# Performance work log

Hardware: AMD Instinct MI355X
Metric: run time of the kernel (lower is better)

## Reference

```python
import jax, jax.numpy as jnp
import numpy as np

D = 1024
H = 16
DK = D // H

def setup_inputs() -> dict:
    key = jax.random.key(0)
    k1, k2, k3 = jax.random.split(key, 3)
    x = jax.random.normal(k1, (2, 2048, D), dtype=jnp.float32)
    # torch nn.Linear weight shapes: qkv [3D, D], o [D, D]; y = x @ W.T
    scale = 1.0 / np.sqrt(D)
    W_qkv = jax.random.normal(k2, (3 * D, D), dtype=jnp.float32) * scale
    W_o = jax.random.normal(k3, (D, D), dtype=jnp.float32) * scale
    return {"x": x, "W_qkv": W_qkv, "W_o": W_o}

def reference(x, W_qkv, W_o):
    B, T, _ = x.shape
    qkv = x @ W_qkv.T                                    # [B, T, 3D]
    qkv = qkv.reshape(B, T, 3, H, DK)
    qkv = jnp.transpose(qkv, (0, 3, 2, 1, 4))            # [B, H, 3, T, DK]
    q, k, v = qkv[:, :, 0], qkv[:, :, 1], qkv[:, :, 2]   # each [B, H, T, DK]
    scores = jnp.einsum("bhqd,bhkd->bhqk", q, k) / np.sqrt(DK)
    causal = jnp.tril(jnp.ones((T, T), dtype=bool))       # keep lower triangle
    scores = jnp.where(causal, scores, -jnp.inf)
    attn = jax.nn.softmax(scores, axis=-1)
    out = jnp.einsum("bhqk,bhkd->bhqd", attn, v)          # [B, H, T, DK]
    out = jnp.transpose(out, (0, 2, 1, 3)).reshape(B, T, H * DK)
    return out @ W_o.T
```

## Files before the change

kernel.cpp:

```cpp
#include <hip/hip_runtime.h>
#include <hip/hip_bf16.h>

typedef __bf16 bf16x8 __attribute__((ext_vector_type(8)));
typedef float f32x4 __attribute__((ext_vector_type(4)));
typedef unsigned int u32;
typedef u32 u32x4 __attribute__((ext_vector_type(4)));

#define MFMA(a, b, c) __builtin_amdgcn_mfma_f32_16x16x32_bf16((a), (b), (c), 0, 0, 0)

static __device__ __forceinline__ bf16x8 ld8(const __bf16* p) {
  return *reinterpret_cast<const bf16x8*>(p);
}

static __device__ __forceinline__ u32 pkbf(float a, float b) {
  union { __bf16 h; unsigned short s; } x, y;
  x.h = (__bf16)a; y.h = (__bf16)b;
  return (u32)x.s | ((u32)y.s << 16);
}

typedef unsigned int __attribute__((address_space(1))) gu32_t;
typedef unsigned int __attribute__((address_space(3))) lu32_t;
static __device__ __forceinline__ void gld16(const __bf16* g, __bf16* l) {
  __builtin_amdgcn_global_load_lds((const gu32_t*)(const void*)g,
                                   (lu32_t*)(void*)l, 16, 0, 0);
}

__global__ __launch_bounds__(256)
void cvt_f32_bf16(const float* __restrict__ a, __bf16* __restrict__ oa, int na,
                  const float* __restrict__ b, __bf16* __restrict__ ob) {
  const int i = blockIdx.x * 256 + threadIdx.x;
  const float* src; __bf16* dst; int e;
  if (i < (na >> 3)) { src = a; dst = oa; e = i << 3; }
  else { src = b; dst = ob; e = (i << 3) - na; }
  f32x4 v0 = *reinterpret_cast<const f32x4*>(src + e);
  f32x4 v1 = *reinterpret_cast<const f32x4*>(src + e + 4);
  bf16x8 o;
#pragma unroll
  for (int j = 0; j < 4; ++j) { o[j] = (__bf16)v0[j]; o[j + 4] = (__bf16)v1[j]; }
  *reinterpret_cast<bf16x8*>(dst + e) = o;
}

static __device__ __forceinline__ void stage8f(__bf16* __restrict__ dst,
                                               const float* __restrict__ src) {
  f32x4 a = *reinterpret_cast<const f32x4*>(src);
  f32x4 b = *reinterpret_cast<const f32x4*>(src + 4);
  bf16x8 o;
#pragma unroll
  for (int i = 0; i < 4; ++i) { o[i] = (__bf16)a[i]; o[i + 4] = (__bf16)b[i]; }
  *reinterpret_cast<bf16x8*>(dst) = o;
}

template<int BN, bool SPLIT, bool OUT_BF16, bool B_F32>
__global__ __launch_bounds__(256, 2)
void gemm3(const __bf16* __restrict__ A, const void* __restrict__ Wv,
           void* __restrict__ Cv, __bf16* __restrict__ VT,
           int M, int N, int K) {
  constexpr int NF = BN / 32;
  constexpr float SC2Q = 0.125f * 1.4426950408889634f;
  __shared__ __bf16 lA[128 * 64];
  __shared__ __bf16 lB[BN * 64];

  const int tid = threadIdx.x;
  const int ntiles = N / BN;
  const int per = gridDim.x >> 3;
  const int bid = (blockIdx.x & 7) * per + (blockIdx.x >> 3);
  const int mt = bid / ntiles;
  const int nt = bid % ntiles;
  const int m0 = mt << 7, n0 = nt * BN;
  const int lane = tid & 63, w = tid >> 6;
  const int wm = (w >> 1) << 6;
  const int wn = (w & 1) * (BN / 2);
  const int fr = lane & 15, fg = lane >> 4;

  f32x4 acc[4][NF] = {};

  for (int k0 = 0; k0 < K; k0 += 64) {
    __syncthreads();
#pragma unroll
    for (int jj = 0; jj < 4; ++jj) {
      const int q = (w << 2) | jj;
      const int v = (q << 6) | lane;
      const int row = v >> 3;
      const int cc = (v & 7) ^ (row & 7);
      gld16(A + (size_t)(m0 + row) * K + k0 + (cc << 3), lA + (q << 9));
    }
    if constexpr (B_F32) {
#pragma unroll
      for (int hh = 0; hh < BN / 64; ++hh) {
        const int row = (tid >> 2) + (hh << 6);
        const int c0 = (tid & 3) << 1;
        const float* src = (const float*)Wv + (size_t)(n0 + row) * K + k0 + (c0 << 3);
#pragma unroll
        for (int cg = 0; cg < 2; ++cg)
          stage8f(lB + (row << 6) + (((c0 + cg) ^ (row & 7)) << 3), src + (cg << 3));
      }
    } else {
#pragma unroll
      for (int jj = 0; jj < NF; ++jj) {
        const int q = w * NF + jj;
        const int v = (q << 6) | lane;
        const int row = v >> 3;
        const int cc = (v & 7) ^ (row & 7);
        gld16((const __bf16*)Wv + (size_t)(n0 + row) * K + k0 + (cc << 3), lB + (q << 9));
      }
    }
    __syncthreads();

    bf16x8 af[2][4], bfr[2][NF];
#pragma unroll
    for (int kc = 0; kc < 2; ++kc) {
#pragma unroll
      for (int m = 0; m < 4; ++m) {
        const int row = wm + m * 16 + fr;
        af[kc][m] = ld8(lA + (row << 6) + ((((kc << 2) | fg) ^ (row & 7)) << 3));
      }
#pragma unroll
      for (int n = 0; n < NF; ++n) {
        const int row = wn + n * 16 + fr;
        bfr[kc][n] = ld8(lB + (row << 6) + ((((kc << 2) | fg) ^ (row & 7)) << 3));
      }
    }
#pragma unroll
    for (int kc = 0; kc < 2; ++kc)
#pragma unroll
      for (int m = 0; m < 4; ++m)
#pragma unroll
        for (int n = 0; n < NF; ++n)
          acc[m][n] = MFMA(af[kc][m], bfr[kc][n], acc[m][n]);
  }

#pragma unroll
  for (int m = 0; m < 4; ++m) {
#pragma unroll
    for (int n = 0; n < NF; ++n) {
#pragma unroll
      for (int r = 0; r < 4; ++r) {
        int row = m0 + wm + m * 16 + fg * 4 + r;
        int col = n0 + wn + n * 16 + fr;
        float v = acc[m][n][r];
        if constexpr (SPLIT) {
          int b = row >> 11, t = row & 2047;
          if (col >= 2048) {
            VT[((size_t)(b << 10) + (col - 2048)) * 2048 + t] = (__bf16)v;
          } else {
            if (col < 1024) v *= SC2Q;
            ((__bf16*)Cv)[(size_t)row * 2048 + col] = (__bf16)v;
          }
        } else if constexpr (OUT_BF16) {
          ((__bf16*)Cv)[(size_t)row * N + col] = (__bf16)v;
        } else {
          ((float*)Cv)[(size_t)row * N + col] = v;
        }
      }
    }
  }
}

static __device__ __forceinline__ void softmax_step(
    f32x4 (&s)[4], f32x4 (&o)[4], float& m, float& l, bf16x8 (&pa)[2],
    bool diag, int q0wt, int k0, int fg, int fr) {
  constexpr float NEG = -1e30f;
  float sv[4][4];
#pragma unroll
  for (int n = 0; n < 4; ++n)
#pragma unroll
    for (int r = 0; r < 4; ++r) {
      float x = s[n][r];
      if (diag && (k0 + n * 16 + fg * 4 + r > q0wt + fr)) x = NEG;
      sv[n][r] = x;
    }

  float t0 = fmaxf(fmaxf(sv[0][0], sv[0][1]), fmaxf(sv[0][2], sv[0][3]));
  float t1 = fmaxf(fmaxf(sv[1][0], sv[1][1]), fmaxf(sv[1][2], sv[1][3]));
  float t2 = fmaxf(fmaxf(sv[2][0], sv[2][1]), fmaxf(sv[2][2], sv[2][3]));
  float t3 = fmaxf(fmaxf(sv[3][0], sv[3][1]), fmaxf(sv[3][2], sv[3][3]));
  float rm = fmaxf(fmaxf(t0, t1), fmaxf(t2, t3));
  rm = fmaxf(rm, __shfl_xor(rm, 16));
  rm = fmaxf(rm, __shfl_xor(rm, 32));

  if (!__all(rm <= m + 16.f)) {
    float mnew = fmaxf(m, rm);
    float alpha = __builtin_exp2f(m - mnew);
    m = mnew;
    l *= alpha;
    float ao[4];
#pragma unroll
    for (int r = 0; r < 4; ++r)
      ao[r] = __shfl(alpha, fg * 4 + r);
#pragma unroll
    for (int n = 0; n < 4; ++n)
#pragma unroll
      for (int r = 0; r < 4; ++r)
        o[n][r] *= ao[r];
  }

  float p[4][4];
#pragma unroll
  for (int n = 0; n < 4; ++n)
#pragma unroll
    for (int r = 0; r < 4; ++r)
      p[n][r] = __builtin_exp2f(sv[n][r] - m);

  float u0 = (p[0][0] + p[0][1]) + (p[0][2] + p[0][3]);
  float u1 = (p[1][0] + p[1][1]) + (p[1][2] + p[1][3]);
  float u2 = (p[2][0] + p[2][1]) + (p[2][2] + p[2][3]);
  float u3 = (p[3][0] + p[3][1]) + (p[3][2] + p[3][3]);
  float rs = (u0 + u1) + (u2 + u3);
  rs += __shfl_xor(rs, 16);
  rs += __shfl_xor(rs, 32);
  l += rs;

  u32 wpk[4][2];
#pragma unroll
  for (int n = 0; n < 4; ++n) {
    wpk[n][0] = pkbf(p[n][0], p[n][1]);
    wpk[n][1] = pkbf(p[n][2], p[n][3]);
  }

  u32 rcv[2][2][2];
#pragma unroll
  for (int e = 0; e < 2; ++e) {
    const int src = fr + ((((fg & 1) << 1) | ((fg >> 1) ^ e)) << 4);
    const bool tsel = ((fg & 1) ^ e) != 0;
#pragma unroll
    for (int c = 0; c < 2; ++c)
#pragma unroll
      for (int hh = 0; hh < 2; ++hh) {
        u32 v = tsel ? wpk[(c << 1) | 1][hh] : wpk[(c << 1) | 0][hh];
        rcv[e][c][hh] = (u32)__shfl((int)v, src);
      }
  }
  const bool hi = (fg >> 1) != 0;
  u32x4 w0, w1;
#pragma unroll
  for (int a = 0; a < 2; ++a)
#pragma unroll
    for (int hh = 0; hh < 2; ++hh) {
      w0[2 * a + hh] = hi ? rcv[a ^ 1][0][hh] : rcv[a][0][hh];
      w1[2 * a + hh] = hi ? rcv[a ^ 1][1][hh] : rcv[a][1][hh];
    }
  pa[0] = __builtin_bit_cast(bf16x8, w0);
  pa[1] = __builtin_bit_cast(bf16x8, w1);
}

static __device__ __forceinline__ void write_out(
    __bf16* __restrict__ out, f32x4 (&o)[4], float l,
    int b, int hoff, int q0wt, int fg, int fr) {
  float linv = 1.f / l;
  float lo[4];
#pragma unroll
  for (int r = 0; r < 4; ++r)
    lo[r] = __shfl(linv, fg * 4 + r);
#pragma unroll
  for (int n = 0; n < 4; ++n)
#pragma unroll
    for (int r = 0; r < 4; ++r) {
      int t = q0wt + fg * 4 + r;
      out[((size_t)(b * 2048 + t)) * 1024 + hoff + n * 16 + fr] = (__bf16)(o[n][r] * lo[r]);
    }
}

__global__ __launch_bounds__(256, 4)
void attn_causal10(const __bf16* __restrict__ qk, const __bf16* __restrict__ vt,
                   __bf16* __restrict__ out) {
  constexpr float NEG = -1e30f;

  __shared__ __bf16 lK[2][4096];
  __shared__ __bf16 lV[2][4096];

  const int tid = threadIdx.x;
  const int lane = tid & 63, w = tid >> 6;
  const int fr = lane & 15, fg = lane >> 4;
  const int blk = blockIdx.x;
  const int j = blk >> 3;
  const int bh = ((blk & 7) << 2) | (j & 3);
  const int qb = 31 - (j >> 2);
  const int b = bh >> 4, h = bh & 15;
  const int q0w = (qb << 6) + (w << 4);
  const int hoff = h * 64;
  const size_t qkbase = (size_t)b * (2048 * 2048);
  const __bf16* kb = qk + qkbase + 1024 + hoff;
  const __bf16* vtb = vt + (size_t)((b << 10) | hoff) * 2048;

  bf16x8 qf[2];
#pragma unroll
  for (int c = 0; c < 2; ++c)
    qf[c] = ld8(qk + qkbase + (size_t)(q0w + fr) * 2048 + hoff + c * 32 + fg * 8);

  f32x4 o[4] = {};
  float m = NEG;
  float l = 0.f;

#define STAGE(bf, k0s)                                                        \
  do {                                                                        \
    _Pragma("unroll")                                                         \
    for (int jj = 0; jj < 2; ++jj) {                                          \
      const int q = (w << 1) | jj;                                            \
      const int v = (q << 6) | lane;                                          \
      const int row = v >> 3;                                                 \
      const int cc = (v & 7) ^ (row & 7);                                     \
      gld16(kb + (size_t)((k0s) + row) * 2048 + (cc << 3), &lK[bf][q << 9]);  \
      gld16(vtb + (size_t)row * 2048 + (k0s) + (cc << 3), &lV[bf][q << 9]);   \
    }                                                                         \
  } while (0)

  int buf = 0;
  STAGE(0, 0);
  __syncthreads();

  for (int kt = 0; kt <= qb; ++kt) {
    const int k0 = kt << 6;
    if (kt < qb) STAGE(buf ^ 1, k0 + 64);

    f32x4 s[4] = {};
#pragma unroll
    for (int c = 0; c < 2; ++c) {
      bf16x8 kfc[4];
#pragma unroll
      for (int n = 0; n < 4; ++n) {
        const int row = n * 16 + fr;
        const int sc = ((c << 2) | fg) ^ (row & 7);
        kfc[n] = ld8(&lK[buf][(row << 6) + (sc << 3)]);
      }
#pragma unroll
      for (int n = 0; n < 4; ++n)
        s[n] = MFMA(kfc[n], qf[c], s[n]);
    }

    bf16x8 pa[2];
    softmax_step(s, o, m, l, pa, kt == qb, q0w, k0, fg, fr);

#pragma unroll
    for (int c = 0; c < 2; ++c) {
      bf16x8 vfc[4];
#pragma unroll
      for (int n = 0; n < 4; ++n) {
        const int row = n * 16 + fr;
        const int sc = ((c << 2) | fg) ^ (row & 7);
        vfc[n] = ld8(&lV[buf][(row << 6) + (sc << 3)]);
      }
#pragma unroll
      for (int n = 0; n < 4; ++n)
        o[n] = MFMA(pa[c], vfc[n], o[n]);
    }

    __syncthreads();
    buf ^= 1;
  }
#undef STAGE

  write_out(out, o, l, b, hoff, q0w, fg, fr);
}

extern "C" void kernel_launch(void* const* d_in, const int* in_sizes, int n_in,
                              void* d_out, int out_size, void* d_ws, size_t ws_size,
                              hipStream_t stream) {
  const float* x = (const float*)d_in[0];
  const float* w_qkv = (const float*)d_in[1];
  const float* w_o = (const float*)d_in[2];
  float* out = (float*)d_out;

  const int M = 4096;
  __bf16* qk = (__bf16*)d_ws;
  __bf16* vt = (__bf16*)((char*)d_ws + (size_t)M * 2048 * 2);
  __bf16* attn = (__bf16*)((char*)d_ws + (size_t)M * 3072 * 2);

  __bf16* xb = (__bf16*)d_out;
  __bf16* wqb = xb + 4194304;
  const int NX = 4194304;

  cvt_f32_bf16<<<3584, 256, 0, stream>>>(x, xb, NX, w_qkv, wqb);

  gemm3<128, true, true, false><<<(M / 128) * (3072 / 128), 256, 0, stream>>>(
      xb, (const void*)wqb, (void*)qk, vt, M, 3072, 1024);

  attn_causal10<<<1024, 256, 0, stream>>>(qk, vt, attn);

  gemm3<64, false, false, true><<<(M / 128) * (1024 / 64), 256, 0, stream>>>(
      attn, (const void*)w_o, (void*)out, nullptr, M, 1024, 1024);
}
```

Measured before the change: 119.3 us.

## Split longest causal query blocks across two workgroups and merge with combine kernel

The 8 heaviest query blocks per (b,h) are split into two workgroups that process interleaved (even/odd) key tiles. Each half writes a normalized partial output plus a log-sum-exp statistic, and a new combine kernel merges them with softmax weights. The goal is to shorten the critical-path tail of the causal workload and to balance work across the 1280 workgroups, and the occupancy hint is raised to 5 waves. In exchange it adds an extra kernel launch, extra global traffic for the partials, and bf16 rounding of the partial outputs before they are combined.

```diff
diff --git a/kernel.cpp b/kernel.cpp
--- a/kernel.cpp
+++ b/kernel.cpp
@@ -260,9 +260,10 @@
     }
 }
 
-__global__ __launch_bounds__(256, 4)
-void attn_causal10(const __bf16* __restrict__ qk, const __bf16* __restrict__ vt,
-                   __bf16* __restrict__ out) {
+__global__ __launch_bounds__(256, 5)
+void attn_causal16(const __bf16* __restrict__ qk, const __bf16* __restrict__ vt,
+                   __bf16* __restrict__ attn, __bf16* __restrict__ pb1,
+                   float* __restrict__ sbuf) {
   constexpr float NEG = -1e30f;
 
   __shared__ __bf16 lK[2][4096];
@@ -272,9 +273,14 @@
   const int lane = tid & 63, w = tid >> 6;
   const int fr = lane & 15, fg = lane >> 4;
   const int blk = blockIdx.x;
-  const int j = blk >> 3;
-  const int bh = ((blk & 7) << 2) | (j & 3);
-  const int qb = 31 - (j >> 2);
+  const int bh = ((blk & 7) << 2) | ((blk >> 3) & 3);
+  const int jb = blk >> 5;
+  int qb, p0, st;
+  bool split;
+  if (jb < 8) { qb = 23 - jb; p0 = 0; st = 1; split = false; }
+  else if (jb < 24) { int sj = jb - 8; qb = 31 - (sj >> 1); p0 = sj & 1; st = 2; split = true; }
+  else { qb = 15 - (jb - 24); p0 = 0; st = 1; split = false; }
+
   const int b = bh >> 4, h = bh & 15;
   const int q0w = (qb << 6) + (w << 4);
   const int hoff = h * 64;
@@ -305,12 +311,12 @@
   } while (0)
 
   int buf = 0;
-  STAGE(0, 0);
+  STAGE(0, p0 << 6);
   __syncthreads();
 
-  for (int kt = 0; kt <= qb; ++kt) {
+  for (int kt = p0; kt <= qb; kt += st) {
     const int k0 = kt << 6;
-    if (kt < qb) STAGE(buf ^ 1, k0 + 64);
+    if (kt + st <= qb) STAGE(buf ^ 1, (kt + st) << 6);
 
     f32x4 s[4] = {};
 #pragma unroll
@@ -349,7 +355,57 @@
   }
 #undef STAGE
 
-  write_out(out, o, l, b, hoff, q0w, fg, fr);
+  if (!split) {
+    write_out(attn, o, l, b, hoff, q0w, fg, fr);
+  } else {
+    const int ti = ((31 - qb) << 5) | bh;
+    const float s_stat = m + __log2f(l);
+    if (p0 == 0) {
+      write_out(attn, o, l, b, hoff, q0w, fg, fr);
+      if (fg == 0) sbuf[ti * 64 + w * 16 + fr] = s_stat;
+    } else {
+      float linv = 1.f / l;
+      float lo[4];
+#pragma unroll
+      for (int r = 0; r < 4; ++r)
+        lo[r] = __shfl(linv, fg * 4 + r);
+#pragma unroll
+      for (int n = 0; n < 4; ++n)
+#pragma unroll
+        for (int r = 0; r < 4; ++r)
+          pb1[(size_t)ti * 4096 + (w * 16 + fg * 4 + r) * 64 + n * 16 + fr] =
+              (__bf16)(o[n][r] * lo[r]);
+      if (fg == 0) sbuf[16384 + ti * 64 + w * 16 + fr] = s_stat;
+    }
+  }
+}
+
+__global__ __launch_bounds__(256)
+void attn_combine16(const __bf16* __restrict__ pb1, const float* __restrict__ sbuf,
+                    __bf16* __restrict__ attn) {
+  const int u = blockIdx.x * 256 + threadIdx.x;
+  const int ti = u >> 9;
+  const int rw = (u >> 3) & 63;
+  const int d8 = (u & 7) << 3;
+  const int qb = 31 - (ti >> 5), bh = ti & 31;
+  const int b = bh >> 4, h = bh & 15;
+  const int t = (qb << 6) + rw;
+
+  const float s0 = sbuf[ti * 64 + rw];
+  const float s1 = sbuf[16384 + ti * 64 + rw];
+  const float sm = fmaxf(s0, s1);
+  float w0 = __builtin_exp2f(s0 - sm), w1 = __builtin_exp2f(s1 - sm);
+  const float inv = 1.f / (w0 + w1);
+  w0 *= inv; w1 *= inv;
+
+  __bf16* dst = attn + ((size_t)(b * 2048 + t)) * 1024 + h * 64 + d8;
+  bf16x8 a = ld8(dst);
+  bf16x8 c = ld8(pb1 + (size_t)ti * 4096 + rw * 64 + d8);
+  bf16x8 o;
+#pragma unroll
+  for (int e = 0; e < 8; ++e)
+    o[e] = (__bf16)(w0 * (float)a[e] + w1 * (float)c[e]);
+  *reinterpret_cast<bf16x8*>(dst) = o;
 }
 
 extern "C" void kernel_launch(void* const* d_in, const int* in_sizes, int n_in,
@@ -364,9 +420,11 @@
   __bf16* qk = (__bf16*)d_ws;
   __bf16* vt = (__bf16*)((char*)d_ws + (size_t)M * 2048 * 2);
   __bf16* attn = (__bf16*)((char*)d_ws + (size_t)M * 3072 * 2);
+  float* sbuf = (float*)((char*)d_ws + 33554432);
 
   __bf16* xb = (__bf16*)d_out;
   __bf16* wqb = xb + 4194304;
+  __bf16* pb1 = wqb + 3145728;
   const int NX = 4194304;
 
   cvt_f32_bf16<<<3584, 256, 0, stream>>>(x, xb, NX, w_qkv, wqb);
@@ -374,7 +432,9 @@
   gemm3<128, true, true, false><<<(M / 128) * (3072 / 128), 256, 0, stream>>>(
       xb, (const void*)wqb, (void*)qk, vt, M, 3072, 1024);
 
-  attn_causal10<<<1024, 256, 0, stream>>>(qk, vt, attn);
+  attn_causal16<<<1280, 256, 0, stream>>>(qk, vt, attn, pb1, sbuf);
+
+  attn_combine16<<<512, 256, 0, stream>>>(pb1, sbuf, attn);
 
   gemm3<64, false, false, true><<<(M / 128) * (1024 / 64), 256, 0, stream>>>(
       attn, (const void*)w_o, (void*)out, nullptr, M, 1024, 1024);
```

Measured after the change: 129.2 us. 8.3% more time.
